# Kernel tuning notes

Hardware: AMD Instinct MI355X
Metric: run time of the kernel (lower is better)

## Reference

```python
import jax, jax.numpy as jnp
import numpy as np

B, S, E = 64, 512, 1024
H = 16
D = E // H  # 64

def setup_inputs() -> dict:
    key = jax.random.key(0)
    ks = jax.random.split(key, 5)
    scale = 1.0 / np.sqrt(E)
    return {
        "hidden_states": jax.random.normal(ks[0], (B, S, E), dtype=jnp.float32),
        "Wq": jax.random.normal(ks[1], (E, E), dtype=jnp.float32) * scale,
        "Wk": jax.random.normal(ks[2], (E, E), dtype=jnp.float32) * scale,
        "Wv": jax.random.normal(ks[3], (E, E), dtype=jnp.float32) * scale,
        "Wo": jax.random.normal(ks[4], (E, E), dtype=jnp.float32) * scale,
        "bo": jnp.zeros((E,), dtype=jnp.float32),
    }

def reference(hidden_states, Wq, Wk, Wv, Wo, bo):
    b, s, e = hidden_states.shape
    # projections (bias-free), split heads -> [B, H, S, D]
    def split(x):
        return x.reshape(b, s, H, D).transpose(0, 2, 1, 3)
    q = split(hidden_states @ Wq)
    k = split(hidden_states @ Wk)
    v = split(hidden_states @ Wv)
    # NOTE: original module applies NO 1/sqrt(d) scaling
    scores = jnp.einsum('bhqd,bhkd->bhqk', q.astype(jnp.float32), k.astype(jnp.float32))
    causal = jnp.tril(jnp.ones((s, s), dtype=bool))  # [S, S]
    mask_value = jnp.finfo(scores.dtype).min
    scores = jnp.where(causal[None, None, :, :], scores, mask_value)
    attn = jax.nn.softmax(scores, axis=-1).astype(v.dtype)
    out = jnp.einsum('bhqk,bhkd->bhqd', attn, v)  # [B, H, S, D]
    out = out.transpose(0, 2, 1, 3).reshape(b, s, e)  # merge heads
    out = out @ Wo + bo
    return out
```

## Files before the change

### kernel.cpp

```cpp
#include <hip/hip_runtime.h>
#include <hip/hip_bf16.h>
#include <cstdint>
#include <cstddef>

#define B_ 64
#define S_ 512
#define E_ 1024
#define H_ 16
#define D_ 64

typedef __attribute__((ext_vector_type(8))) short s8v;
typedef __attribute__((ext_vector_type(4))) float f4v;

__device__ __forceinline__ ushort f2bf(float f) {
  uint32_t u = __builtin_bit_cast(uint32_t, f);
  u += 0x7fffu + ((u >> 16) & 1u);
  return (ushort)(u >> 16);
}

__device__ __forceinline__ void async_cp16(const void* g, void* l) {
  __builtin_amdgcn_global_load_lds(
      (const __attribute__((address_space(1))) unsigned int*)g,
      (__attribute__((address_space(3))) unsigned int*)(uintptr_t)l,
      16, 0, 0);
}

__global__ __launch_bounds__(256) void convertx(const float* __restrict__ X,
                                                ushort* __restrict__ Y) {
  size_t i = ((size_t)blockIdx.x * 256 + threadIdx.x) * 4;
  float4 v = *(const float4*)(X + i);
  uint2 p;
  p.x = (uint32_t)f2bf(v.x) | ((uint32_t)f2bf(v.y) << 16);
  p.y = (uint32_t)f2bf(v.z) | ((uint32_t)f2bf(v.w) << 16);
  *(uint2*)(Y + i) = p;
}

__global__ __launch_bounds__(256) void transpose_w(const float* __restrict__ W,
                                                   ushort* __restrict__ Wt) {
  __shared__ ushort T[32][33];
  int x = threadIdx.x & 31, y = threadIdx.x >> 5;
  int c0 = blockIdx.x * 32;
  int r0 = blockIdx.y * 32;
#pragma unroll
  for (int i = 0; i < 4; i++) {
    int r = y + i * 8;
    T[x][r] = f2bf(W[(size_t)(r0 + r) * E_ + c0 + x]);
  }
  __syncthreads();
#pragma unroll
  for (int i = 0; i < 4; i++) {
    int r = y + i * 8;
    Wt[(size_t)(c0 + r) * E_ + r0 + x] = T[r][x];
  }
}

__device__ __forceinline__ void gemm256_core(const ushort* __restrict__ A,
                                             const ushort* __restrict__ Bt,
                                             int m0, int n0, ushort* smem,
                                             f4v acc[8][4]) {
  const int tid = threadIdx.x;
  const int wave = tid >> 6, lane = tid & 63;
  const int wm = wave >> 2, wn = wave & 3;
  const int lrow = lane & 15, quad = lane >> 4;
  const int sw = (lrow & 3) ^ ((lrow >> 2) & 3);
  const int aoff = (wm * 128 + lrow) * 32 + (quad ^ sw) * 8;
  const int boff = (wn * 64 + lrow) * 32 + (quad ^ sw) * 8;
  const int sr = tid >> 2;
  const int sc = ((tid & 3) ^ (sr & 3) ^ ((sr >> 2) & 3)) * 8;
  const ushort* Ab = A + (size_t)m0 * E_;
  const ushort* Bb = Bt + (size_t)n0 * E_;

#define SA_(buf, kh) (smem + ((buf) * 2 + (kh)) * 8192)
#define SB_(buf, kh) (smem + 32768 + ((buf) * 2 + (kh)) * 8192)

  auto STG = [&](const ushort* g, ushort* l) {
    async_cp16(g + (size_t)sr * E_ + sc, l + tid * 8);
    async_cp16(g + (size_t)(sr + 128) * E_ + sc, l + 4096 + tid * 8);
  };

#pragma unroll
  for (int i = 0; i < 8; i++)
#pragma unroll
    for (int j = 0; j < 4; j++) acc[i][j] = (f4v){0.f, 0.f, 0.f, 0.f};

  STG(Ab + 0, SA_(0, 0));
  STG(Bb + 0, SB_(0, 0));
  STG(Ab + 32, SA_(0, 1));
  STG(Bb + 32, SB_(0, 1));
  STG(Ab + 64, SA_(1, 0));
  STG(Bb + 64, SB_(1, 0));
  asm volatile("s_waitcnt vmcnt(8)" ::: "memory");
  __builtin_amdgcn_s_barrier();

  for (int t = 0; t < 16; ++t) {
    const int buf = t & 1;
    const ushort* A0s = SA_(buf, 0);
    const ushort* A1s = SA_(buf, 1);
    const ushort* B0s = SB_(buf, 0);
    const ushort* B1s = SB_(buf, 1);
    s8v a[4], b[4];

#pragma unroll
    for (int i = 0; i < 4; i++) a[i] = *(const s8v*)(A0s + aoff + i * 512);
#pragma unroll
    for (int i = 0; i < 4; i++) b[i] = *(const s8v*)(B0s + boff + i * 512);
    if (t < 15) STG(Ab + (size_t)(t + 1) * 64 + 32, SA_(buf ^ 1, 1));
    __builtin_amdgcn_s_barrier();
    __builtin_amdgcn_s_setprio(1);
#pragma unroll
    for (int i = 0; i < 4; i++)
#pragma unroll
      for (int n = 0; n < 4; n++)
        acc[i][n] = __builtin_amdgcn_mfma_f32_16x16x32_bf16(a[i], b[n], acc[i][n], 0, 0, 0);
    __builtin_amdgcn_s_setprio(0);
    __builtin_amdgcn_s_barrier();

#pragma unroll
    for (int i = 0; i < 4; i++) a[i] = *(const s8v*)(A0s + aoff + (4 + i) * 512);
    if (t < 15) {
      STG(Bb + (size_t)(t + 1) * 64 + 32, SB_(buf ^ 1, 1));
      asm volatile("s_waitcnt vmcnt(8)" ::: "memory");
    } else {
      asm volatile("s_waitcnt vmcnt(0)" ::: "memory");
    }
    __builtin_amdgcn_s_barrier();
    __builtin_amdgcn_s_setprio(1);
#pragma unroll
    for (int i = 0; i < 4; i++)
#pragma unroll
      for (int n = 0; n < 4; n++)
        acc[4 + i][n] = __builtin_amdgcn_mfma_f32_16x16x32_bf16(a[i], b[n], acc[4 + i][n], 0, 0, 0);
    __builtin_amdgcn_s_setprio(0);
    __builtin_amdgcn_s_barrier();

#pragma unroll
    for (int i = 0; i < 4; i++) a[i] = *(const s8v*)(A1s + aoff + i * 512);
#pragma unroll
    for (int i = 0; i < 4; i++) b[i] = *(const s8v*)(B1s + boff + i * 512);
    if (t < 14) STG(Ab + (size_t)(t + 2) * 64, SA_(buf, 0));
    __builtin_amdgcn_s_barrier();
    __builtin_amdgcn_s_setprio(1);
#pragma unroll
    for (int i = 0; i < 4; i++)
#pragma unroll
      for (int n = 0; n < 4; n++)
        acc[i][n] = __builtin_amdgcn_mfma_f32_16x16x32_bf16(a[i], b[n], acc[i][n], 0, 0, 0);
    __builtin_amdgcn_s_setprio(0);
    __builtin_amdgcn_s_barrier();

#pragma unroll
    for (int i = 0; i < 4; i++) a[i] = *(const s8v*)(A1s + aoff + (4 + i) * 512);
    if (t < 14) {
      STG(Bb + (size_t)(t + 2) * 64, SB_(buf, 0));
      asm volatile("s_waitcnt vmcnt(8)" ::: "memory");
    } else if (t == 14) {
      asm volatile("s_waitcnt vmcnt(4)" ::: "memory");
    }
    __builtin_amdgcn_s_barrier();
    __builtin_amdgcn_s_setprio(1);
#pragma unroll
    for (int i = 0; i < 4; i++)
#pragma unroll
      for (int n = 0; n < 4; n++)
        acc[4 + i][n] = __builtin_amdgcn_mfma_f32_16x16x32_bf16(a[i], b[n], acc[4 + i][n], 0, 0, 0);
    __builtin_amdgcn_s_setprio(0);
    __builtin_amdgcn_s_barrier();
  }
#undef SA_
#undef SB_
}

__global__ __launch_bounds__(512, 2) void gemm_qkv(
    const ushort* __restrict__ A, const ushort* __restrict__ Bt,
    ushort* __restrict__ Qo, ushort* __restrict__ Ko, ushort* __restrict__ Vt) {
  __shared__ __align__(16) ushort smem[65536];
  const int orig = blockIdx.x;
  const int swz = (orig & 7) * 192 + (orig >> 3);
  const int ntile = swz % 12, mtile = swz / 12;
  const int n0 = ntile * 256, m0 = mtile * 256;

  f4v acc[8][4];
  gemm256_core(A, Bt, m0, n0, smem, acc);

  const int tid = threadIdx.x;
  const int wave = tid >> 6, lane = tid & 63;
  const int wm = wave >> 2, wn = wave & 3;
  const int lrow = lane & 15, quad = lane >> 4;
  const int proj = n0 >> 10;
  const int np0 = n0 & 1023;
  const int hb = np0 >> 6;
  const int bb = m0 >> 9, s0 = m0 & 511;

  if (proj < 2) {
    ushort* C = proj == 0 ? Qo : Ko;
#pragma unroll
    for (int h = 0; h < 2; h++) {
#pragma unroll
      for (int mf = 0; mf < 4; mf++)
#pragma unroll
        for (int n = 0; n < 4; n++)
#pragma unroll
          for (int r = 0; r < 4; r++)
            smem[(wm * 64 + mf * 16 + quad * 4 + r) * 264 + wn * 64 + n * 16 + lrow] =
                f2bf(acc[h * 4 + mf][n][r]);
      __syncthreads();
#pragma unroll
      for (int j = 0; j < 8; j++) {
        int chunk = j * 512 + tid;
        int pr = chunk >> 5, cc = chunk & 31;
        int s = s0 + (pr >> 6) * 128 + h * 64 + (pr & 63);
        int hd = hb + (cc >> 3);
        size_t off = (((size_t)bb * H_ + hd) * S_ + s) * D_ + (cc & 7) * 8;
        *(uint4*)&C[off] = *(const uint4*)&smem[pr * 264 + cc * 8];
      }
      if (h == 0) __syncthreads();
    }
  } else {
#pragma unroll
    for (int w = 0; w < 2; w++) {
      if (wm == w) {
#pragma unroll
        for (int m = 0; m < 8; m++)
#pragma unroll
          for (int n = 0; n < 4; n++) {
            ushort4 pk;
            pk.x = f2bf(acc[m][n][0]);
            pk.y = f2bf(acc[m][n][1]);
            pk.z = f2bf(acc[m][n][2]);
            pk.w = f2bf(acc[m][n][3]);
            *(ushort4*)&smem[(wn * 64 + n * 16 + lrow) * 136 + m * 16 + quad * 4] = pk;
          }
      }
      __syncthreads();
#pragma unroll
      for (int j = 0; j < 8; j++) {
        int chunk = j * 512 + tid;
        int dr = chunk >> 4, cc = chunk & 15;
        int hd = hb + (dr >> 6), d = dr & 63;
        size_t off = (((size_t)bb * H_ + hd) * D_ + d) * S_ + s0 + w * 128 + cc * 8;
        *(uint4*)&Vt[off] = *(const uint4*)&smem[dr * 136 + cc * 8];
      }
      if (w == 0) __syncthreads();
    }
  }
}

__global__ __launch_bounds__(512, 2) void gemm_o(
    const ushort* __restrict__ A, const ushort* __restrict__ Bt,
    float* __restrict__ C, const float* __restrict__ bias) {
  __shared__ __align__(16) ushort smem[65536];
  const int orig = blockIdx.x;
  const int swz = (orig & 7) * 64 + (orig >> 3);
  const int ntile = swz & 3, mtile = swz >> 2;
  const int n0 = ntile * 256, m0 = mtile * 256;

  f4v acc[8][4];
  gemm256_core(A, Bt, m0, n0, smem, acc);

  const int tid = threadIdx.x;
  const int wave = tid >> 6, lane = tid & 63;
  const int wm = wave >> 2, wn = wave & 3;
  const int lrow = lane & 15, quad = lane >> 4;
#pragma unroll
  for (int n = 0; n < 4; n++) {
    int col = n0 + wn * 64 + n * 16 + lrow;
    float bv = bias[col];
#pragma unroll
    for (int m = 0; m < 8; m++) {
      int row = m0 + wm * 128 + m * 16 + quad * 4;
#pragma unroll
      for (int r = 0; r < 4; r++)
        C[(size_t)(row + r) * E_ + col] = acc[m][n][r] + bv;
    }
  }
}

__global__ __launch_bounds__(256, 3) void attn_kernel(
    const ushort* __restrict__ Qg, const ushort* __restrict__ Kg,
    const ushort* __restrict__ Vtg, ushort* __restrict__ AO) {
  __shared__ __align__(16) ushort Ks[2][64 * 64];
  __shared__ __align__(16) ushort Vts[2][64 * 64];
  __shared__ __align__(16) ushort Ps[4][32 * 72];

  const int qp = blockIdx.x;
  const int bh = blockIdx.y;
  const int b = bh >> 4, h = bh & 15;
  const int tid = threadIdx.x, wave = tid >> 6, lane = tid & 63;
  const int lrow = lane & 15, quad = lane >> 4;
  const int swl = lrow & 7;
  const size_t base = (size_t)bh * (S_ * D_);
  const int qB0 = qp * 64 + wave * 16;
  const int qB1 = (7 - qp) * 64 + wave * 16;
  const int kd0 = qp, kd1 = 7 - qp;
  const int NT = kd1 + 1;

  s8v qf[2][2];
#pragma unroll
  for (int kk = 0; kk < 2; kk++) {
    qf[0][kk] = *(const s8v*)(Qg + base + (size_t)(qB0 + lrow) * 64 + kk * 32 + quad * 8);
    qf[1][kk] = *(const s8v*)(Qg + base + (size_t)(qB1 + lrow) * 64 + kk * 32 + quad * 8);
  }

  f4v o[2][4];
#pragma unroll
  for (int mi = 0; mi < 2; mi++)
#pragma unroll
    for (int di = 0; di < 4; di++) o[mi][di] = (f4v){0.f, 0.f, 0.f, 0.f};
  float mr[2] = {-INFINITY, -INFINITY};
  float lr[2] = {0.f, 0.f};

  ushort* pw = &Ps[wave][0];

  auto STAGE = [&](int kt, int bf) {
#pragma unroll
    for (int i = 0; i < 2; i++) {
      int c = i * 256 + tid;
      int r = c >> 3, cc = c & 7;
      int sc = cc ^ (r & 7);
      async_cp16(Kg + base + (size_t)(kt * 64 + r) * 64 + sc * 8, (void*)&Ks[bf][c * 8]);
    }
#pragma unroll
    for (int i = 0; i < 2; i++) {
      int c = i * 256 + tid;
      int d = c >> 3, cc = c & 7;
      int sc = cc ^ (d & 7);
      async_cp16(Vtg + base + (size_t)d * S_ + kt * 64 + sc * 8, (void*)&Vts[bf][c * 8]);
    }
  };

  STAGE(0, 0);
  __syncthreads();

  int buf = 0;
  for (int kt = 0; kt < NT; kt++) {
    if (kt + 1 < NT) STAGE(kt + 1, buf ^ 1);
    const bool act0 = (kt <= kd0);
    const ushort* Kb = &Ks[buf][0];
    const ushort* Vb = &Vts[buf][0];

    f4v st[2][4];
#pragma unroll
    for (int mi = 0; mi < 2; mi++)
#pragma unroll
      for (int ni = 0; ni < 4; ni++) st[mi][ni] = (f4v){0.f, 0.f, 0.f, 0.f};
    __builtin_amdgcn_s_setprio(1);
#pragma unroll
    for (int kk = 0; kk < 2; kk++) {
      const int ch = (kk * 4 + quad) ^ swl;
#pragma unroll
      for (int ni = 0; ni < 4; ni++) {
        s8v kf = *(const s8v*)&Kb[(ni * 16 + lrow) * 64 + ch * 8];
        st[1][ni] = __builtin_amdgcn_mfma_f32_16x16x32_bf16(kf, qf[1][kk], st[1][ni], 0, 0, 0);
        if (act0)
          st[0][ni] = __builtin_amdgcn_mfma_f32_16x16x32_bf16(kf, qf[0][kk], st[0][ni], 0, 0, 0);
      }
    }
    __builtin_amdgcn_s_setprio(0);

    float alr[2][4];
#pragma unroll
    for (int mi = 0; mi < 2; mi++) {
      if (mi == 0 && !act0) continue;
      const int qB = mi ? qB1 : qB0;
      if (kt == (mi ? kd1 : kd0)) {
        int qrow = qB + lrow;
#pragma unroll
        for (int ni = 0; ni < 4; ni++) {
          int kc0 = kt * 64 + ni * 16 + quad * 4;
#pragma unroll
          for (int r = 0; r < 4; r++)
            if (kc0 + r > qrow) st[mi][ni][r] = -INFINITY;
        }
      }
      float bm = st[mi][0][0];
#pragma unroll
      for (int ni = 0; ni < 4; ni++)
#pragma unroll
        for (int r = 0; r < 4; r++) bm = fmaxf(bm, st[mi][ni][r]);
      bm = fmaxf(bm, __shfl_xor(bm, 16));
      bm = fmaxf(bm, __shfl_xor(bm, 32));
      float mn = fmaxf(mr[mi], bm);
      float al = __expf(mr[mi] - mn);
      mr[mi] = mn;
      float bs = 0.f;
#pragma unroll
      for (int ni = 0; ni < 4; ni++) {
        float p0 = __expf(st[mi][ni][0] - mn);
        float p1 = __expf(st[mi][ni][1] - mn);
        float p2 = __expf(st[mi][ni][2] - mn);
        float p3 = __expf(st[mi][ni][3] - mn);
        bs += (p0 + p1) + (p2 + p3);
        ushort4 pk = {f2bf(p0), f2bf(p1), f2bf(p2), f2bf(p3)};
        *(ushort4*)&pw[(mi * 16 + lrow) * 72 + ni * 16 + quad * 4] = pk;
      }
      bs += __shfl_xor(bs, 16);
      bs += __shfl_xor(bs, 32);
      lr[mi] = lr[mi] * al + bs;
#pragma unroll
      for (int r = 0; r < 4; r++) alr[mi][r] = __shfl(al, (lane & 48) + quad * 4 + r);
#pragma unroll
      for (int di = 0; di < 4; di++)
#pragma unroll
        for (int r = 0; r < 4; r++) o[mi][di][r] *= alr[mi][r];
    }

    __builtin_amdgcn_s_setprio(1);
#pragma unroll
    for (int kk = 0; kk < 2; kk++) {
      const int ch = (kk * 4 + quad) ^ swl;
      s8v pf1 = *(const s8v*)&pw[(16 + lrow) * 72 + kk * 32 + quad * 8];
      if (act0) {
        s8v pf0 = *(const s8v*)&pw[lrow * 72 + kk * 32 + quad * 8];
#pragma unroll
        for (int di = 0; di < 4; di++) {
          s8v vf = *(const s8v*)&Vb[(di * 16 + lrow) * 64 + ch * 8];
          o[1][di] = __builtin_amdgcn_mfma_f32_16x16x32_bf16(pf1, vf, o[1][di], 0, 0, 0);
          o[0][di] = __builtin_amdgcn_mfma_f32_16x16x32_bf16(pf0, vf, o[0][di], 0, 0, 0);
        }
      } else {
#pragma unroll
        for (int di = 0; di < 4; di++) {
          s8v vf = *(const s8v*)&Vb[(di * 16 + lrow) * 64 + ch * 8];
          o[1][di] = __builtin_amdgcn_mfma_f32_16x16x32_bf16(pf1, vf, o[1][di], 0, 0, 0);
        }
      }
    }
    __builtin_amdgcn_s_setprio(0);

    __syncthreads();
    buf ^= 1;
  }

  float inv[2][4];
#pragma unroll
  for (int mi = 0; mi < 2; mi++)
#pragma unroll
    for (int r = 0; r < 4; r++)
      inv[mi][r] = 1.0f / __shfl(lr[mi], (lane & 48) + quad * 4 + r);

#pragma unroll
  for (int mi = 0; mi < 2; mi++)
#pragma unroll
    for (int di = 0; di < 4; di++)
#pragma unroll
      for (int r = 0; r < 4; r++)
        pw[(mi * 16 + quad * 4 + r) * 72 + di * 16 + lrow] = f2bf(o[mi][di][r] * inv[mi][r]);

#pragma unroll
  for (int i = 0; i < 4; i++) {
    int c = i * 64 + lane;
    int row = c >> 3, cc = c & 7;
    uint4 val = *(const uint4*)&pw[row * 72 + cc * 8];
    int q = ((row >> 4) ? qB1 : qB0) + (row & 15);
    size_t off = ((size_t)b * S_ + q) * E_ + h * 64 + cc * 8;
    *(uint4*)&AO[off] = val;
  }
}

extern "C" void kernel_launch(void* const* d_in, const int* in_sizes, int n_in,
                              void* d_out, int out_size, void* d_ws, size_t ws_size,
                              hipStream_t stream) {
  const float* X = (const float*)d_in[0];
  const float* Wq = (const float*)d_in[1];
  const float* Wk = (const float*)d_in[2];
  const float* Wv = (const float*)d_in[3];
  const float* Wo = (const float*)d_in[4];
  const float* bo = (const float*)d_in[5];
  float* out = (float*)d_out;

  char* ws = (char*)d_ws;
  ushort* Xb = (ushort*)(ws);
  ushort* Wqkvt = (ushort*)(ws + 67108864);
  ushort* Wot = (ushort*)(ws + 73400320);
  ushort* Qb = (ushort*)(ws + 75497472);
  ushort* Kb = (ushort*)(ws + 142606336);
  ushort* Vtb = (ushort*)(ws + 209715200);
  ushort* AO = Xb;

  convertx<<<32768, 256, 0, stream>>>(X, Xb);
  transpose_w<<<dim3(32, 32), 256, 0, stream>>>(Wq, Wqkvt);
  transpose_w<<<dim3(32, 32), 256, 0, stream>>>(Wk, Wqkvt + 1024 * 1024);
  transpose_w<<<dim3(32, 32), 256, 0, stream>>>(Wv, Wqkvt + 2 * 1024 * 1024);
  transpose_w<<<dim3(32, 32), 256, 0, stream>>>(Wo, Wot);

  gemm_qkv<<<1536, 512, 0, stream>>>(Xb, Wqkvt, Qb, Kb, Vtb);

  attn_kernel<<<dim3(4, 1024), 256, 0, stream>>>(Qb, Kb, Vtb, AO);

  gemm_o<<<512, 512, 0, stream>>>(AO, Wot, out, bo);
}
```

Baseline: 632.9 us.

## Restructure GEMM LDS tiles to full 64-wide K with 8-chunk swizzle and batched prefetch

The shared-memory layout of the 256x256 GEMM core changes from two 32-wide K halves per buffer to a single 64-wide K row per buffer, using an XOR swizzle over 8 chunks. Global-to-LDS prefetches for the next-but-one K step are issued together after the last MFMA group, instead of being spread across the four sub-phases. This cuts the number of separate async-copy issue points and waitcnt stalls inside the loop, and is meant to improve LDS bank behaviour. In exchange, loads are overlapped with less of the compute, which could expose memory latency.

```diff
diff --git a/kernel.cpp b/kernel.cpp
--- a/kernel.cpp
+++ b/kernel.cpp
@@ -62,20 +62,23 @@
   const int wave = tid >> 6, lane = tid & 63;
   const int wm = wave >> 2, wn = wave & 3;
   const int lrow = lane & 15, quad = lane >> 4;
-  const int sw = (lrow & 3) ^ ((lrow >> 2) & 3);
-  const int aoff = (wm * 128 + lrow) * 32 + (quad ^ sw) * 8;
-  const int boff = (wn * 64 + lrow) * 32 + (quad ^ sw) * 8;
-  const int sr = tid >> 2;
-  const int sc = ((tid & 3) ^ (sr & 3) ^ ((sr >> 2) & 3)) * 8;
+  const int swl = lrow & 7;
+  const int ch0 = (quad ^ swl) * 8;
+  const int ch1 = ((4 + quad) ^ swl) * 8;
+  const int arow = (wm * 128 + lrow) * 64;
+  const int brow = (wn * 64 + lrow) * 64;
+  const int rr = tid >> 3;
+  const int sq = ((tid & 7) ^ (rr & 7)) * 8;
   const ushort* Ab = A + (size_t)m0 * E_;
   const ushort* Bb = Bt + (size_t)n0 * E_;
 
-#define SA_(buf, kh) (smem + ((buf) * 2 + (kh)) * 8192)
-#define SB_(buf, kh) (smem + 32768 + ((buf) * 2 + (kh)) * 8192)
+#define SA_(buf) (smem + (buf) * 16384)
+#define SB_(buf) (smem + 32768 + (buf) * 16384)
 
   auto STG = [&](const ushort* g, ushort* l) {
-    async_cp16(g + (size_t)sr * E_ + sc, l + tid * 8);
-    async_cp16(g + (size_t)(sr + 128) * E_ + sc, l + 4096 + tid * 8);
+#pragma unroll
+    for (int i = 0; i < 4; i++)
+      async_cp16(g + (size_t)(rr + i * 64) * E_ + sq, l + i * 4096 + tid * 8);
   };
 
 #pragma unroll
@@ -83,28 +86,23 @@
 #pragma unroll
     for (int j = 0; j < 4; j++) acc[i][j] = (f4v){0.f, 0.f, 0.f, 0.f};
 
-  STG(Ab + 0, SA_(0, 0));
-  STG(Bb + 0, SB_(0, 0));
-  STG(Ab + 32, SA_(0, 1));
-  STG(Bb + 32, SB_(0, 1));
-  STG(Ab + 64, SA_(1, 0));
-  STG(Bb + 64, SB_(1, 0));
+  STG(Ab + 0, SA_(0));
+  STG(Bb + 0, SB_(0));
+  STG(Ab + 64, SA_(1));
+  STG(Bb + 64, SB_(1));
   asm volatile("s_waitcnt vmcnt(8)" ::: "memory");
   __builtin_amdgcn_s_barrier();
 
   for (int t = 0; t < 16; ++t) {
     const int buf = t & 1;
-    const ushort* A0s = SA_(buf, 0);
-    const ushort* A1s = SA_(buf, 1);
-    const ushort* B0s = SB_(buf, 0);
-    const ushort* B1s = SB_(buf, 1);
+    const ushort* As = SA_(buf);
+    const ushort* Bs = SB_(buf);
     s8v a[4], b[4];
 
 #pragma unroll
-    for (int i = 0; i < 4; i++) a[i] = *(const s8v*)(A0s + aoff + i * 512);
-#pragma unroll
-    for (int i = 0; i < 4; i++) b[i] = *(const s8v*)(B0s + boff + i * 512);
-    if (t < 15) STG(Ab + (size_t)(t + 1) * 64 + 32, SA_(buf ^ 1, 1));
+    for (int i = 0; i < 4; i++) a[i] = *(const s8v*)(As + arow + i * 1024 + ch0);
+#pragma unroll
+    for (int n = 0; n < 4; n++) b[n] = *(const s8v*)(Bs + brow + n * 1024 + ch0);
     __builtin_amdgcn_s_barrier();
     __builtin_amdgcn_s_setprio(1);
 #pragma unroll
@@ -116,13 +114,7 @@
     __builtin_amdgcn_s_barrier();
 
 #pragma unroll
-    for (int i = 0; i < 4; i++) a[i] = *(const s8v*)(A0s + aoff + (4 + i) * 512);
-    if (t < 15) {
-      STG(Bb + (size_t)(t + 1) * 64 + 32, SB_(buf ^ 1, 1));
-      asm volatile("s_waitcnt vmcnt(8)" ::: "memory");
-    } else {
-      asm volatile("s_waitcnt vmcnt(0)" ::: "memory");
-    }
+    for (int i = 0; i < 4; i++) a[i] = *(const s8v*)(As + arow + (4 + i) * 1024 + ch0);
     __builtin_amdgcn_s_barrier();
     __builtin_amdgcn_s_setprio(1);
 #pragma unroll
@@ -134,10 +126,9 @@
     __builtin_amdgcn_s_barrier();
 
 #pragma unroll
-    for (int i = 0; i < 4; i++) a[i] = *(const s8v*)(A1s + aoff + i * 512);
-#pragma unroll
-    for (int i = 0; i < 4; i++) b[i] = *(const s8v*)(B1s + boff + i * 512);
-    if (t < 14) STG(Ab + (size_t)(t + 2) * 64, SA_(buf, 0));
+    for (int i = 0; i < 4; i++) a[i] = *(const s8v*)(As + arow + i * 1024 + ch1);
+#pragma unroll
+    for (int n = 0; n < 4; n++) b[n] = *(const s8v*)(Bs + brow + n * 1024 + ch1);
     __builtin_amdgcn_s_barrier();
     __builtin_amdgcn_s_setprio(1);
 #pragma unroll
@@ -149,21 +140,22 @@
     __builtin_amdgcn_s_barrier();
 
 #pragma unroll
-    for (int i = 0; i < 4; i++) a[i] = *(const s8v*)(A1s + aoff + (4 + i) * 512);
+    for (int i = 0; i < 4; i++) a[i] = *(const s8v*)(As + arow + (4 + i) * 1024 + ch1);
+    __builtin_amdgcn_s_barrier();
+    __builtin_amdgcn_s_setprio(1);
+#pragma unroll
+    for (int i = 0; i < 4; i++)
+#pragma unroll
+      for (int n = 0; n < 4; n++)
+        acc[4 + i][n] = __builtin_amdgcn_mfma_f32_16x16x32_bf16(a[i], b[n], acc[4 + i][n], 0, 0, 0);
+    __builtin_amdgcn_s_setprio(0);
     if (t < 14) {
-      STG(Bb + (size_t)(t + 2) * 64, SB_(buf, 0));
+      STG(Ab + (size_t)(t + 2) * 64, SA_(buf));
+      STG(Bb + (size_t)(t + 2) * 64, SB_(buf));
       asm volatile("s_waitcnt vmcnt(8)" ::: "memory");
     } else if (t == 14) {
-      asm volatile("s_waitcnt vmcnt(4)" ::: "memory");
-    }
-    __builtin_amdgcn_s_barrier();
-    __builtin_amdgcn_s_setprio(1);
-#pragma unroll
-    for (int i = 0; i < 4; i++)
-#pragma unroll
-      for (int n = 0; n < 4; n++)
-        acc[4 + i][n] = __builtin_amdgcn_mfma_f32_16x16x32_bf16(a[i], b[n], acc[4 + i][n], 0, 0, 0);
-    __builtin_amdgcn_s_setprio(0);
+      asm volatile("s_waitcnt vmcnt(0)" ::: "memory");
+    }
     __builtin_amdgcn_s_barrier();
   }
 #undef SA_
```

Measured after the change: 640.1 us. About the same (+1.1%).
